# Kernel tuning notes

Hardware: AMD Instinct MI355X
Metric: run time of the kernel (lower is better)

## Reference

```python
import jax, jax.numpy as jnp
import numpy as np

N, E, C, Z, NB, NG, NL = 4000, 48000, 64, 10, 8, 8, 2
R_MAX = 5.0
P = 5.0  # polynomial cutoff power
AVG_NEIGH = 12.0
# l-index of each of the 16 spherical-harmonic components (l = 0..3)
ELLS = np.concatenate([[0], [1] * 3, [2] * 5, [3] * 7])


def _sph(u):
    # component-normalized real spherical harmonics up to l=3, u: unit vectors [E,3]
    x, y, z = u[..., 0], u[..., 1], u[..., 2]
    s3 = np.sqrt(3.0); s5 = np.sqrt(5.0); s15 = np.sqrt(15.0)
    s7 = np.sqrt(7.0); s105 = np.sqrt(105.0)
    s35_8 = np.sqrt(35.0 / 8.0); s21_8 = np.sqrt(21.0 / 8.0)
    x2, y2, z2 = x * x, y * y, z * z
    return jnp.stack([
        jnp.ones_like(x),
        s3 * x, s3 * y, s3 * z,
        s15 * x * y, s15 * y * z, 0.5 * s5 * (3.0 * z2 - 1.0), s15 * x * z, 0.5 * s15 * (x2 - y2),
        s35_8 * y * (3.0 * x2 - y2), s105 * x * y * z, s21_8 * y * (5.0 * z2 - 1.0),
        0.5 * s7 * z * (5.0 * z2 - 3.0), s21_8 * x * (5.0 * z2 - 1.0),
        0.5 * s105 * z * (x2 - y2), s35_8 * x * (x2 - 3.0 * y2),
    ], axis=-1)


def _radial(r):
    # Bessel radial basis * polynomial cutoff envelope; r: [E,1] -> [E,NB]
    n = jnp.arange(1, NB + 1, dtype=r.dtype)
    bess = np.sqrt(2.0 / R_MAX) * jnp.sin(n * jnp.pi * r / R_MAX) / r
    u = r / R_MAX
    env = 1.0 - 0.5 * (P + 1) * (P + 2) * u ** P + P * (P + 2) * u ** (P + 1) - 0.5 * P * (P + 1) * u ** (P + 2)
    env = jnp.where(u < 1.0, env, 0.0)
    return bess * env


def _per_l(f, W):
    # per-degree (l) channel mixing: f [N,C,16], W [4,C,C]
    return jnp.einsum('ncm,mcd->ndm', f, W[ELLS])


def _model(positions, x, shifts, W_embed, W_up, Wm1, Wm2, Wm3, W_out, W_sc, a_sc, w_poly, W_prod, w_r0, W_r1, w_r2, edge_index, batch):
    sender, receiver = edge_index[0], edge_index[1]
    vec = positions[receiver] - positions[sender] + shifts          # [E,3]
    length = jnp.sqrt(jnp.sum(vec * vec, axis=-1, keepdims=True))   # [E,1]
    edge_attrs = _sph(vec / length)                                 # [E,16]
    edge_feats = _radial(length)                                    # [E,NB]
    nf = jnp.zeros((N, C, 16), positions.dtype).at[:, :, 0].set(x @ W_embed)
    node_e = jnp.zeros((N,), positions.dtype)
    for i in range(NL):
        h = _per_l(nf, W_up[i])                                     # [N,C,16]
        w = jax.nn.silu(edge_feats @ Wm1[i])
        w = jax.nn.silu(w @ Wm2[i])
        w = (w @ Wm3[i]).reshape(E, C, 4)                           # per-(channel,l) radial weights
        h_s = h[:, :, 0][sender][:, :, None]                        # sender scalar feats [E,C,1]
        m = w[:, :, ELLS] * edge_attrs[:, None, :] * h_s            # messages [E,C,16]
        agg = jax.ops.segment_sum(m, receiver, num_segments=N) / AVG_NEIGH
        out = _per_l(agg, W_out[i])
        sc = _per_l(nf, W_sc[i]) * (x @ a_sc[i])[:, :, None]        # element-dependent skip
        s = out[:, :, 0]
        gate = w_poly[i, 0] + w_poly[i, 1] * s + w_poly[i, 2] * s * s  # correlation-3 scalar gate
        nf = _per_l(out * gate[:, :, None], W_prod[i]) + sc
        if i < NL - 1:
            node_e = node_e + nf[:, :, 0] @ w_r0
        else:
            node_e = node_e + jax.nn.silu(nf[:, :, 0] @ W_r1) @ w_r2
    snap = jax.ops.segment_sum(node_e, batch, num_segments=NG)
    return snap, node_e


def setup_inputs() -> dict:
    key = jax.random.key(0)
    ks = jax.random.split(key, 20)
    positions = jax.random.normal(ks[0], (N, 3), jnp.float32) * 3.0
    species = jax.random.randint(ks[1], (N,), 0, Z)
    x = jax.nn.one_hot(species, Z, dtype=jnp.float32)
    sender = jax.random.randint(ks[2], (E,), 0, N)
    offset = jax.random.randint(ks[3], (E,), 1, N)
    receiver = (sender + offset) % N  # no self loops -> length > 0
    edge_index = jnp.stack([sender, receiver]).astype(jnp.int32)
    shifts = jnp.zeros((E, 3), jnp.float32)
    batch = jnp.sort(jax.random.randint(ks[4], (N,), 0, NG)).astype(jnp.int32)
    g = lambda k, shp, scale: jax.random.normal(k, shp, jnp.float32) * scale
    inv = 1.0 / np.sqrt(C)
    return {
        'positions': positions, 'x': x, 'shifts': shifts,
        'W_embed': g(ks[5], (Z, C), 1.0 / np.sqrt(Z)),
        'W_up': g(ks[6], (NL, 4, C, C), inv),
        'Wm1': g(ks[7], (NL, NB, 64), 1.0 / np.sqrt(NB)),
        'Wm2': g(ks[8], (NL, 64, 64), 0.125),
        'Wm3': g(ks[9], (NL, 64, 4 * C), 0.125),
        'W_out': g(ks[10], (NL, 4, C, C), inv),
        'W_sc': g(ks[11], (NL, 4, C, C), inv),
        'a_sc': g(ks[12], (NL, Z, C), 1.0),
        'w_poly': g(ks[13], (NL, 3, C), 0.5),
        'W_prod': g(ks[14], (NL, 4, C, C), inv),
        'w_r0': g(ks[15], (C,), inv),
        'W_r1': g(ks[16], (C, 16), inv),
        'w_r2': g(ks[17], (16,), 0.25),
        'edge_index': edge_index, 'batch': batch,
    }


def reference(positions, x, shifts, W_embed, W_up, Wm1, Wm2, Wm3, W_out, W_sc, a_sc, w_poly, W_prod, w_r0, W_r1, w_r2, edge_index, batch):
    def efn(pos):
        snap, node_e = _model(pos, x, shifts, W_embed, W_up, Wm1, Wm2, Wm3, W_out, W_sc, a_sc, w_poly, W_prod, w_r0, W_r1, w_r2, edge_index, batch)
        return jnp.sum(snap), (snap, node_e)
    (_, (snap, node_e)), g = jax.value_and_grad(efn, has_aux=True)(positions)
    forces = -g
    return snap, node_e, forces
```

## Files before the change

kernel.cpp:

```cpp
#include <hip/hip_runtime.h>
#include <math.h>

constexpr int NN = 4000;
constexpr int EE = 48000;
constexpr int ZZ = 10;
constexpr float RMAX = 5.0f;
constexpr float INV_AVG = 1.0f / 12.0f;

constexpr int ZERO_F4 = (3*NN*64 + 3*NN + 4) / 4;

__device__ __forceinline__ float rl(float v, int lane){
    return __uint_as_float(__builtin_amdgcn_readlane(__float_as_uint(v), lane));
}
__device__ __forceinline__ float sigf(float x){ return 1.0f/(1.0f+__expf(-x)); }
__device__ __forceinline__ float siluf(float x){ return x*sigf(x); }
__device__ __forceinline__ float dsiluf(float x){ float s=sigf(x); return s*(1.0f+x*(1.0f-s)); }

__device__ __forceinline__ void pin64(float (&W)[64]){
#pragma unroll
    for (int i=0;i<64;i++) asm volatile("" : "+v"(W[i]));
}
__device__ __forceinline__ void pin8(float (&W)[8]){
#pragma unroll
    for (int i=0;i<8;i++) asm volatile("" : "+v"(W[i]));
}

__device__ __forceinline__ float bmv64(float src, const float (&W)[64]){
    float a0=0.f,a1=0.f,a2=0.f,a3=0.f;
#pragma unroll
    for (int k=0;k<64;k+=4){
        a0 += rl(src,k+0)*W[k+0];
        a1 += rl(src,k+1)*W[k+1];
        a2 += rl(src,k+2)*W[k+2];
        a3 += rl(src,k+3)*W[k+3];
    }
    return (a0+a1)+(a2+a3);
}
__device__ __forceinline__ void load_row64(const float* __restrict__ p, float (&W)[64]){
#pragma unroll
    for (int i=0;i<16;i++){
        float4 v = reinterpret_cast<const float4*>(p)[i];
        W[4*i]=v.x; W[4*i+1]=v.y; W[4*i+2]=v.z; W[4*i+3]=v.w;
    }
}
__device__ __forceinline__ void load_col64(const float* __restrict__ p, int lane, float (&W)[64]){
#pragma unroll
    for (int k=0;k<64;k++) W[k] = p[k*64+lane];
}

__global__ void k_zero(float4* __restrict__ z, float* __restrict__ out)
{
    int i = blockIdx.x*256 + threadIdx.x;
    if (i < ZERO_F4) z[i] = make_float4(0.f,0.f,0.f,0.f);
    if (blockIdx.x==0 && threadIdx.x<8) out[threadIdx.x] = 0.0f;
}

__global__ void k_geom(const float* __restrict__ pos, const float* __restrict__ shifts,
                       const int* __restrict__ ei, const float* __restrict__ x,
                       const float* __restrict__ WE, const float* __restrict__ W_up,
                       const float* __restrict__ W_sc, const float* __restrict__ a_sc,
                       const float* __restrict__ Wm3,
                       int* __restrict__ spec,
                       float* __restrict__ u3c, float* __restrict__ frc, float* __restrict__ dfrc,
                       int* __restrict__ esrc, int* __restrict__ edst, int* __restrict__ ecount,
                       float* __restrict__ T0, float* __restrict__ SC0, float* __restrict__ W3z)
{
    int b = blockIdx.x;
    if (b >= 236){
        int wv = (b-236)*4 + (threadIdx.x>>6);
        int lane = threadIdx.x & 63;
        if (wv < ZZ){
            float wev = WE[wv*64 + lane];
            float t=0.f, sc=0.f;
#pragma unroll
            for (int c=0;c<64;c++){
                float w = rl(wev,c);
                t  += w*W_up[c*64+lane];
                sc += w*W_sc[c*64+lane];
            }
            T0[wv*64+lane]  = t;
            SC0[wv*64+lane] = sc * a_sc[wv*64+lane];
        }
        return;
    }
    if (b >= 204){
        int idx = (b-204)*256 + threadIdx.x;
        int l = idx >> 12;
        int kc = idx & 4095;
        int k = kc >> 6, c = kc & 63;
        W3z[idx] = Wm3[l*64*256 + k*256 + 4*c];
        return;
    }
    if (b >= 188){
        int n = (b-188)*256 + threadIdx.x;
        if (n < NN){
            int sp = 0;
#pragma unroll
            for (int j=0;j<ZZ;j++) if (x[n*ZZ+j] > 0.5f) sp = j;
            spec[n] = sp;
        }
        return;
    }
    int e = b*256 + threadIdx.x;
    if (e >= EE) return;
    int s = ei[e], r = ei[EE+e];
    float vx = pos[r*3+0]-pos[s*3+0]+shifts[e*3+0];
    float vy = pos[r*3+1]-pos[s*3+1]+shifts[e*3+1];
    float vz = pos[r*3+2]-pos[s*3+2]+shifts[e*3+2];
    float rr = sqrtf(vx*vx+vy*vy+vz*vz);
    float u = rr*(1.0f/RMAX);
    if (u >= 1.0f) return;
    int slot = atomicAdd(ecount, 1);
    esrc[slot]=s; edst[slot]=r;
    float inv = 1.0f/rr;
    u3c[slot*3+0]=vx*inv; u3c[slot*3+1]=vy*inv; u3c[slot*3+2]=vz*inv;
    float u2=u*u, u4=u2*u2, u5=u4*u;
    float env  = 1.0f - 21.0f*u5 + 35.0f*u5*u - 15.0f*u5*u2;
    float om   = 1.0f-u;
    float denv = -21.0f*u4*om*om;
    const float A = 0.6324555320336759f;
    const float K1 = 3.14159265358979f/RMAX;
    float a  = K1*rr;
    float s1 = __sinf(a), c1 = __cosf(a);
    float sp = 0.0f, cp = 1.0f, sn = s1, cn = c1;
#pragma unroll
    for (int n=1;n<=8;n++){
        float k = (float)n*K1;
        float bess  = A*sn*inv;
        float dbess = A*(k*cn - sn*inv)*inv;
        frc [slot*8+n-1] = bess*env;
        dfrc[slot*8+n-1] = dbess*env + bess*denv;
        float s2 = 2.0f*c1*sn - sp; sp=sn; sn=s2;
        float c2 = 2.0f*c1*cn - cp; cp=cn; cn=c2;
    }
}

template<int L>
__global__ __launch_bounds__(256,3)
void k_edge_fwd(const float* __restrict__ frc, const int* __restrict__ esrc,
                const int* __restrict__ edst, const int* __restrict__ ecount,
                const int* __restrict__ spec, const float* __restrict__ T0,
                const float* __restrict__ h1,
                const float* __restrict__ W1, const float* __restrict__ W2,
                const float* __restrict__ W3z,
                float* __restrict__ agg, float* __restrict__ t2b,
                float* __restrict__ w0b)
{
    int lane = threadIdx.x & 63;
    int wid  = (blockIdx.x*256 + threadIdx.x) >> 6;
    int nw   = gridDim.x*4;
    int cnt  = ecount[0];
    float W1c[8], W2c[64], W3c[64];
#pragma unroll
    for (int j=0;j<8;j++) W1c[j] = W1[j*64+lane];
    load_col64(W2,  lane, W2c);
    load_col64(W3z, lane, W3c);
    pin8(W1c); pin64(W2c); pin64(W3c);
    for (int slot=wid; slot<cnt; slot+=nw){
        int us = __builtin_amdgcn_readfirstlane(slot);
        int s = esrc[us], r = edst[us];
        float fv = frc[us*8 + (lane&7)];
        float t1=0.f;
#pragma unroll
        for (int j=0;j<8;j++) t1 += rl(fv,j)*W1c[j];
        float a1v = siluf(t1);
        float t2  = bmv64(a1v, W2c);
        t2b[(size_t)us*64+lane] = t2;
        float a2v = siluf(t2);
        float w0  = bmv64(a2v, W3c);
        if (L==1) w0b[(size_t)us*64+lane] = w0;
        float h = (L==0) ? T0[spec[s]*64+lane] : h1[s*64+lane];
        atomicAdd(&agg[r*64+lane], w0*h*INV_AVG);
    }
}

__global__ __launch_bounds__(256,2)
void k_node_fwd0(const float* __restrict__ agg, const float* __restrict__ SC0,
                 const int* __restrict__ spec, const float* __restrict__ Wout,
                 const float* __restrict__ Wprod, const float* __restrict__ Wup1,
                 const float* __restrict__ poly, const float* __restrict__ wr0,
                 float* __restrict__ s0, float* __restrict__ nf1,
                 float* __restrict__ h1, float* __restrict__ nodee)
{
    int lane = threadIdx.x & 63;
    int wid = (blockIdx.x*256 + threadIdx.x) >> 6;
    int nw  = gridDim.x*4;
    float Oc[64], Pc[64], Uc[64];
    load_col64(Wout, lane, Oc);
    load_col64(Wprod,lane, Pc);
    load_col64(Wup1, lane, Uc);
    pin64(Oc); pin64(Pc); pin64(Uc);
    float p0=poly[lane], p1=poly[64+lane], p2=poly[128+lane];
    float w0r = wr0[lane];
    for (int nn=wid; nn<NN; nn+=nw){
        int n = __builtin_amdgcn_readfirstlane(nn);
        float av = agg[n*64+lane];
        float s  = bmv64(av, Oc);
        float gate = p0 + p1*s + p2*s*s;
        float v  = s*gate;
        float nf = bmv64(v, Pc) + SC0[spec[n]*64+lane];
        s0 [n*64+lane] = s;
        nf1[n*64+lane] = nf;
        h1 [n*64+lane] = bmv64(nf, Uc);
        float ne = nf*w0r;
#pragma unroll
        for (int off=32;off;off>>=1) ne += __shfl_xor(ne,off);
        if (lane==0) nodee[n] = ne;
    }
}

__global__ __launch_bounds__(256,2)
void k_node_fwd1(const float* __restrict__ agg, const float* __restrict__ nf1,
                 const int* __restrict__ spec, const float* __restrict__ Wout,
                 const float* __restrict__ Wprod, const float* __restrict__ Wsc,
                 const float* __restrict__ asc, const float* __restrict__ poly,
                 float* __restrict__ s1, float* __restrict__ nf2)
{
    int lane = threadIdx.x & 63;
    int wid = (blockIdx.x*256 + threadIdx.x) >> 6;
    int nw  = gridDim.x*4;
    float Oc[64], Pc[64], Sc[64];
    load_col64(Wout, lane, Oc);
    load_col64(Wprod,lane, Pc);
    load_col64(Wsc,  lane, Sc);
    pin64(Oc); pin64(Pc); pin64(Sc);
    float p0=poly[lane], p1=poly[64+lane], p2=poly[128+lane];
    for (int nn=wid; nn<NN; nn+=nw){
        int n = __builtin_amdgcn_readfirstlane(nn);
        float av  = agg[n*64+lane];
        float nfv = nf1[n*64+lane];
        float s   = bmv64(av, Oc);
        float gate = p0 + p1*s + p2*s*s;
        float v   = s*gate;
        float scp = bmv64(nfv, Sc);
        float nf  = bmv64(v, Pc) + scp*asc[spec[n]*64+lane];
        s1 [n*64+lane] = s;
        nf2[n*64+lane] = nf;
    }
}

__global__ __launch_bounds__(256,3)
void k_read1(const float* __restrict__ nf2, const float* __restrict__ Wr1,
             const float* __restrict__ wr2, float* __restrict__ nodee,
             float* __restrict__ gnf2)
{
    int lane = threadIdx.x & 63;
    int wid = (blockIdx.x*256 + threadIdx.x) >> 6;
    int nw  = gridDim.x*4;
    int j = lane & 15;
    float Wcol[64];
#pragma unroll
    for (int c=0;c<64;c++) Wcol[c] = Wr1[c*16 + j];
    pin64(Wcol);
    float Wrow[16];
#pragma unroll
    for (int i=0;i<4;i++){
        float4 v = reinterpret_cast<const float4*>(Wr1 + lane*16)[i];
        Wrow[4*i]=v.x; Wrow[4*i+1]=v.y; Wrow[4*i+2]=v.z; Wrow[4*i+3]=v.w;
    }
    float w2 = wr2[j];
    for (int nn=wid; nn<NN; nn+=nw){
        int n = __builtin_amdgcn_readfirstlane(nn);
        float nv = nf2[n*64+lane];
        float z  = bmv64(nv, Wcol);
        float ne = siluf(z)*w2;
#pragma unroll
        for (int off=32;off;off>>=1) ne += __shfl_xor(ne,off);
        ne *= 0.25f;
        float gz = w2*dsiluf(z);
        float g = 0.f;
#pragma unroll
        for (int jj=0;jj<16;jj++) g += rl(gz,jj)*Wrow[jj];
        gnf2[n*64+lane] = g;
        if (lane==0) nodee[n] += ne;
    }
}

__global__ __launch_bounds__(256,2)
void k_bnode1(const float* __restrict__ gin, const float* __restrict__ sbuf,
              const float* __restrict__ Wout, const float* __restrict__ Wprod,
              const float* __restrict__ Wsc, const float* __restrict__ asc,
              const int* __restrict__ spec, const float* __restrict__ poly,
              float* __restrict__ gagg, float* __restrict__ gsc)
{
    int lane = threadIdx.x & 63;
    int wid = (blockIdx.x*256 + threadIdx.x) >> 6;
    int nw  = gridDim.x*4;
    float Pr[64], Or[64], Sr[64];
    load_row64(Wprod + lane*64, Pr);
    load_row64(Wout  + lane*64, Or);
    load_row64(Wsc   + lane*64, Sr);
    pin64(Pr); pin64(Or); pin64(Sr);
    float p0=poly[lane], p1=poly[64+lane], p2=poly[128+lane];
    for (int nn=wid; nn<NN; nn+=nw){
        int n = __builtin_amdgcn_readfirstlane(nn);
        float g  = gin[n*64+lane];
        float gv = bmv64(g, Pr);
        float s  = sbuf[n*64+lane];
        float gate = p0 + p1*s + p2*s*s;
        float gs = gv*(gate + s*(p1 + 2.0f*p2*s));
        gagg[n*64+lane] = bmv64(gs, Or);
        float ga = g * asc[spec[n]*64+lane];
        gsc[n*64+lane] = bmv64(ga, Sr);
    }
}

__global__ __launch_bounds__(256,2)
void k_bnode0(const float* __restrict__ ghb, const float* __restrict__ gacc,
              const float* __restrict__ Wup1, const float* __restrict__ wr0,
              const float* __restrict__ sbuf, const float* __restrict__ Wout,
              const float* __restrict__ Wprod, const float* __restrict__ poly,
              float* __restrict__ gagg)
{
    int lane = threadIdx.x & 63;
    int wid = (blockIdx.x*256 + threadIdx.x) >> 6;
    int nw  = gridDim.x*4;
    float Ur[64], Pr[64], Or[64];
    load_row64(Wup1 + lane*64, Ur);
    load_row64(Wprod+ lane*64, Pr);
    load_row64(Wout + lane*64, Or);
    pin64(Ur); pin64(Pr); pin64(Or);
    float p0=poly[lane], p1=poly[64+lane], p2=poly[128+lane];
    for (int nn=wid; nn<NN; nn+=nw){
        int n = __builtin_amdgcn_readfirstlane(nn);
        float gh = ghb[n*64+lane];
        float g  = bmv64(gh, Ur) + gacc[n*64+lane] + wr0[lane];
        float gv = bmv64(g, Pr);
        float s  = sbuf[n*64+lane];
        float gate = p0 + p1*s + p2*s*s;
        float gs = gv*(gate + s*(p1 + 2.0f*p2*s));
        gagg[n*64+lane] = bmv64(gs, Or);
    }
}

template<int L>
__global__ __launch_bounds__(256,3)
void k_edge_bwd(const float* __restrict__ frc, const float* __restrict__ dfrc,
                const float* __restrict__ u3c, const int* __restrict__ esrc,
                const int* __restrict__ edst, const int* __restrict__ ecount,
                const int* __restrict__ spec, const float* __restrict__ T0,
                const float* __restrict__ h1, const float* __restrict__ gagg,
                const float* __restrict__ t2b, const float* __restrict__ w0b,
                const float* __restrict__ W1, const float* __restrict__ W2,
                const float* __restrict__ W3z,
                float* __restrict__ ghb, float* __restrict__ gpos)
{
    int lane = threadIdx.x & 63;
    int wid  = (blockIdx.x*256 + threadIdx.x) >> 6;
    int nw   = gridDim.x*4;
    int cnt  = ecount[0];
    float W3r[64], W2r[64], W1c[8];
    load_row64(W3z + lane*64, W3r);
    load_row64(W2  + lane*64, W2r);
#pragma unroll
    for (int j=0;j<8;j++) W1c[j] = W1[j*64+lane];
    pin64(W3r); pin64(W2r); pin8(W1c);
    for (int slot=wid; slot<cnt; slot+=nw){
        int us = __builtin_amdgcn_readfirstlane(slot);
        int s = esrc[us], r = edst[us];
        float gm = gagg[r*64+lane]*INV_AVG;
        float h  = (L==0) ? T0[spec[s]*64+lane] : h1[s*64+lane];
        float gw0 = gm*h;
        if (L==1) atomicAdd(&ghb[s*64+lane], gm*w0b[(size_t)us*64+lane]);
        float ga2 = bmv64(gw0, W3r);
        float t2v = t2b[(size_t)us*64+lane];
        float gt2 = ga2*dsiluf(t2v);
        float ga1 = bmv64(gt2, W2r);
        float fv  = frc [us*8+(lane&7)];
        float dfv = dfrc[us*8+(lane&7)];
        float t1=0.f, wd=0.f;
#pragma unroll
        for (int j=0;j<8;j++){ t1 += rl(fv,j)*W1c[j]; wd += rl(dfv,j)*W1c[j]; }
        float gt1 = ga1*dsiluf(t1);
        float p = gt1*wd;
#pragma unroll
        for (int off=32;off;off>>=1) p += __shfl_xor(p,off);
        if (lane<3) atomicAdd(&gpos[r*3+lane],  u3c[us*3+lane]*p);
        else if (lane>=32 && lane<35){ int d=lane-32; atomicAdd(&gpos[s*3+d], -u3c[us*3+d]*p); }
    }
}

__global__ void k_final(const float* __restrict__ node_e, const int* __restrict__ batch,
                        const float* __restrict__ gpos, float* __restrict__ out)
{
    __shared__ float part[8];
    int tid=threadIdx.x;
    if (tid<8) part[tid]=0.0f;
    __syncthreads();
    int n = blockIdx.x*256 + tid;
    if (n<NN){
        float ne = node_e[n];
        out[8+n] = ne;
        atomicAdd(&part[batch[n]], ne);
        out[8+NN + n*3+0] = -gpos[n*3+0];
        out[8+NN + n*3+1] = -gpos[n*3+1];
        out[8+NN + n*3+2] = -gpos[n*3+2];
    }
    __syncthreads();
    if (tid<8) atomicAdd(&out[tid], part[tid]);
}

extern "C" void kernel_launch(void* const* d_in, const int* in_sizes, int n_in,
                              void* d_out, int out_size, void* d_ws, size_t ws_size,
                              hipStream_t stream)
{
    (void)in_sizes; (void)n_in; (void)out_size; (void)ws_size;
    const float* pos    = (const float*)d_in[0];
    const float* x      = (const float*)d_in[1];
    const float* shifts = (const float*)d_in[2];
    const float* W_embed= (const float*)d_in[3];
    const float* W_up   = (const float*)d_in[4];
    const float* Wm1    = (const float*)d_in[5];
    const float* Wm2    = (const float*)d_in[6];
    const float* Wm3    = (const float*)d_in[7];
    const float* W_out  = (const float*)d_in[8];
    const float* W_sc   = (const float*)d_in[9];
    const float* a_sc   = (const float*)d_in[10];
    const float* w_poly = (const float*)d_in[11];
    const float* W_prod = (const float*)d_in[12];
    const float* w_r0   = (const float*)d_in[13];
    const float* W_r1   = (const float*)d_in[14];
    const float* w_r2   = (const float*)d_in[15];
    const int*   ei     = (const int*)d_in[16];
    const int*   batch  = (const int*)d_in[17];
    float* out = (float*)d_out;

    float* F = (float*)d_ws;
    float* agg0 = F; F += NN*64;
    float* agg1 = F; F += NN*64;
    float* ghb  = F; F += NN*64;
    float* gpos = F; F += NN*3;
    int* ecount = (int*)F; F += 4;
    float* u3c  = F; F += 3*EE;
    float* frc  = F; F += 8*EE;
    float* dfrc = F; F += 8*EE;
    float* t2b0 = F; F += (size_t)EE*64;
    float* t2b1 = F; F += (size_t)EE*64;
    float* w0b1 = F; F += (size_t)EE*64;
    float* h1   = F; F += NN*64;
    float* nf1  = F; F += NN*64;
    float* nf2  = F; F += NN*64;
    float* s0   = F; F += NN*64;
    float* s1   = F; F += NN*64;
    float* nodee= F; F += NN;
    float* gnf2 = F; F += NN*64;
    float* gagg1= F; F += NN*64;
    float* gagg0= F; F += NN*64;
    float* gacc = F; F += NN*64;
    float* T0   = F; F += ZZ*64;
    float* SC0  = F; F += ZZ*64;
    float* W3z  = F; F += 2*64*64;
    int* spec   = (int*)F; F += NN;
    int* esrc   = (int*)F; F += EE;
    int* edst   = (int*)F; F += EE;

    const float* U0 = W_up;           const float* U1 = W_up   + 4*64*64;
    const float* O0 = W_out;          const float* O1 = W_out  + 4*64*64;
    const float* S0w= W_sc;           const float* S1w= W_sc   + 4*64*64;
    const float* P0 = W_prod;         const float* P1 = W_prod + 4*64*64;
    const float* M1_0=Wm1,  *M1_1=Wm1+8*64;
    const float* M2_0=Wm2,  *M2_1=Wm2+64*64;
    const float* asc1=a_sc+ZZ*64;
    const float* pl0=w_poly, *pl1=w_poly+3*64;
    float* W3z0 = W3z; float* W3z1 = W3z + 64*64;

    k_zero<<<(ZERO_F4+255)/256, 256, 0, stream>>>((float4*)d_ws, out);
    k_geom<<<239, 256, 0, stream>>>(pos, shifts, ei, x, W_embed, U0, S0w, a_sc, Wm3,
                                    spec, u3c, frc, dfrc, esrc, edst, ecount, T0, SC0, W3z);

    k_edge_fwd<0><<<768,256,0,stream>>>(frc, esrc, edst, ecount, spec, T0, nullptr,
                                        M1_0, M2_0, W3z0, agg0, t2b0, nullptr);
    k_node_fwd0<<<500,256,0,stream>>>(agg0, SC0, spec, O0, P0, U1, pl0, w_r0,
                                      s0, nf1, h1, nodee);
    k_edge_fwd<1><<<768,256,0,stream>>>(frc, esrc, edst, ecount, spec, nullptr, h1,
                                        M1_1, M2_1, W3z1, agg1, t2b1, w0b1);
    k_node_fwd1<<<500,256,0,stream>>>(agg1, nf1, spec, O1, P1, S1w, asc1, pl1, s1, nf2);
    k_read1<<<500,256,0,stream>>>(nf2, W_r1, w_r2, nodee, gnf2);

    k_bnode1<<<500,256,0,stream>>>(gnf2, s1, O1, P1, S1w, asc1, spec, pl1, gagg1, gacc);
    k_edge_bwd<1><<<768,256,0,stream>>>(frc, dfrc, u3c, esrc, edst, ecount, spec, nullptr, h1,
                                        gagg1, t2b1, w0b1, M1_1, M2_1, W3z1, ghb, gpos);
    k_bnode0<<<500,256,0,stream>>>(ghb, gacc, U1, w_r0, s0, O0, P0, pl0, gagg0);
    k_edge_bwd<0><<<768,256,0,stream>>>(frc, dfrc, u3c, esrc, edst, ecount, spec, T0, nullptr,
                                        gagg0, t2b0, nullptr, M1_0, M2_0, W3z0, nullptr, gpos);

    k_final<<<16,256,0,stream>>>(nodee, batch, gpos, out);
}
```

Baseline: 150.9 us.

## Fuse node kernels, fold zeroing and final pass, recompute layer-0 edge MLP

Several changes land together. Workspace zeroing moves into extra blocks of the geometry kernel, and the final output kernel is removed: forces accumulate straight into the output and node energies reduce per graph inside the node kernels. The layer-1 node forward, readout and backward node kernels merge into one with four nodes per wave. Layer-0 edge backward recomputes the hidden activation instead of storing and reloading a 48000x64 buffer, and edge and node grids shrink. This cuts launches and memory traffic at the cost of extra recompute, higher register pressure and more atomics to the output.

```diff
diff --git a/kernel.cpp b/kernel.cpp
--- a/kernel.cpp
+++ b/kernel.cpp
@@ -7,7 +7,13 @@
 constexpr float RMAX = 5.0f;
 constexpr float INV_AVG = 1.0f / 12.0f;
 
-constexpr int ZERO_F4 = (3*NN*64 + 3*NN + 4) / 4;
+constexpr int GB_EDGE = 188;
+constexpr int GB_SPEC = GB_EDGE + 16;
+constexpr int GB_W3Z  = GB_SPEC + 32;
+constexpr int GB_T0   = GB_W3Z + 3;
+constexpr int GB_ZERO = GB_T0 + 64;
+constexpr int ZWS_F4  = 3*NN*64/4;
+constexpr int ZOUT_F4 = 3*NN/4;
 
 __device__ __forceinline__ float rl(float v, int lane){
     return __uint_as_float(__builtin_amdgcn_readlane(__float_as_uint(v), lane));
@@ -48,11 +54,11 @@
     for (int k=0;k<64;k++) W[k] = p[k*64+lane];
 }
 
-__global__ void k_zero(float4* __restrict__ z, float* __restrict__ out)
-{
-    int i = blockIdx.x*256 + threadIdx.x;
-    if (i < ZERO_F4) z[i] = make_float4(0.f,0.f,0.f,0.f);
-    if (blockIdx.x==0 && threadIdx.x<8) out[threadIdx.x] = 0.0f;
+__global__ void k_zero(int* __restrict__ ecount, float* __restrict__ out)
+{
+    int t = threadIdx.x;
+    if (t < 8) out[t] = 0.0f;
+    if (t == 8) *ecount = 0;
 }
 
 __global__ void k_geom(const float* __restrict__ pos, const float* __restrict__ shifts,
@@ -63,11 +69,25 @@
                        int* __restrict__ spec,
                        float* __restrict__ u3c, float* __restrict__ frc, float* __restrict__ dfrc,
                        int* __restrict__ esrc, int* __restrict__ edst, int* __restrict__ ecount,
-                       float* __restrict__ T0, float* __restrict__ SC0, float* __restrict__ W3z)
+                       float* __restrict__ T0, float* __restrict__ SC0, float* __restrict__ W3z,
+                       float4* __restrict__ zws, float* __restrict__ out)
 {
     int b = blockIdx.x;
-    if (b >= 236){
-        int wv = (b-236)*4 + (threadIdx.x>>6);
+    if (b >= GB_T0){
+        if (b >= GB_ZERO) return;
+        if (b >= GB_W3Z && b < GB_T0){}
+        if (b >= GB_T0 && b < GB_ZERO){
+            float4 z4 = make_float4(0.f,0.f,0.f,0.f);
+            float4* zout = (float4*)(out + 8 + NN);
+            for (int i=(b-GB_T0)*256 + threadIdx.x; i < ZWS_F4 + ZOUT_F4; i += 64*256){
+                if (i < ZWS_F4) zws[i] = z4;
+                else zout[i-ZWS_F4] = z4;
+            }
+            return;
+        }
+    }
+    if (b >= GB_W3Z && b < GB_T0){
+        int wv = (b-GB_W3Z)*4 + (threadIdx.x>>6);
         int lane = threadIdx.x & 63;
         if (wv < ZZ){
             float wev = WE[wv*64 + lane];
@@ -83,16 +103,16 @@
         }
         return;
     }
-    if (b >= 204){
-        int idx = (b-204)*256 + threadIdx.x;
+    if (b >= GB_SPEC && b < GB_W3Z){
+        int idx = (b-GB_SPEC)*256 + threadIdx.x;
         int l = idx >> 12;
         int kc = idx & 4095;
         int k = kc >> 6, c = kc & 63;
         W3z[idx] = Wm3[l*64*256 + k*256 + 4*c];
         return;
     }
-    if (b >= 188){
-        int n = (b-188)*256 + threadIdx.x;
+    if (b >= GB_EDGE){
+        int n = (b-GB_EDGE)*256 + threadIdx.x;
         if (n < NN){
             int sp = 0;
 #pragma unroll
@@ -147,8 +167,8 @@
                 float* __restrict__ w0b)
 {
     int lane = threadIdx.x & 63;
-    int wid  = (blockIdx.x*256 + threadIdx.x) >> 6;
-    int nw   = gridDim.x*4;
+    int wid  = __builtin_amdgcn_readfirstlane((blockIdx.x*256 + threadIdx.x) >> 6);
+    const int nw = 512*4;
     int cnt  = ecount[0];
     float W1c[8], W2c[64], W3c[64];
 #pragma unroll
@@ -165,10 +185,12 @@
         for (int j=0;j<8;j++) t1 += rl(fv,j)*W1c[j];
         float a1v = siluf(t1);
         float t2  = bmv64(a1v, W2c);
-        t2b[(size_t)us*64+lane] = t2;
         float a2v = siluf(t2);
         float w0  = bmv64(a2v, W3c);
-        if (L==1) w0b[(size_t)us*64+lane] = w0;
+        if (L==1){
+            t2b[(size_t)us*64+lane] = t2;
+            w0b[(size_t)us*64+lane] = w0;
+        }
         float h = (L==0) ? T0[spec[s]*64+lane] : h1[s*64+lane];
         atomicAdd(&agg[r*64+lane], w0*h*INV_AVG);
     }
@@ -176,93 +198,91 @@
 
 __global__ __launch_bounds__(256,2)
 void k_node_fwd0(const float* __restrict__ agg, const float* __restrict__ SC0,
-                 const int* __restrict__ spec, const float* __restrict__ Wout,
-                 const float* __restrict__ Wprod, const float* __restrict__ Wup1,
-                 const float* __restrict__ poly, const float* __restrict__ wr0,
+                 const int* __restrict__ spec, const int* __restrict__ batch,
+                 const float* __restrict__ Wout, const float* __restrict__ Wprod,
+                 const float* __restrict__ Wup1, const float* __restrict__ poly,
+                 const float* __restrict__ wr0,
                  float* __restrict__ s0, float* __restrict__ nf1,
-                 float* __restrict__ h1, float* __restrict__ nodee)
-{
+                 float* __restrict__ h1, float* __restrict__ out)
+{
+    __shared__ float part[8];
+    if (threadIdx.x < 8) part[threadIdx.x] = 0.f;
+    __syncthreads();
     int lane = threadIdx.x & 63;
-    int wid = (blockIdx.x*256 + threadIdx.x) >> 6;
-    int nw  = gridDim.x*4;
-    float Oc[64], Pc[64], Uc[64];
-    load_col64(Wout, lane, Oc);
-    load_col64(Wprod,lane, Pc);
-    load_col64(Wup1, lane, Uc);
-    pin64(Oc); pin64(Pc); pin64(Uc);
+    int wid = __builtin_amdgcn_readfirstlane((blockIdx.x*256 + threadIdx.x) >> 6);
+    float WA[64], WB[64], WC[64];
+    load_col64(Wout, lane, WA);
+    load_col64(Wprod,lane, WB);
+    load_col64(Wup1, lane, WC);
+    pin64(WA); pin64(WB); pin64(WC);
     float p0=poly[lane], p1=poly[64+lane], p2=poly[128+lane];
     float w0r = wr0[lane];
-    for (int nn=wid; nn<NN; nn+=nw){
-        int n = __builtin_amdgcn_readfirstlane(nn);
+#pragma unroll
+    for (int i=0;i<4;i++){
+        int n = wid + i*1000;
         float av = agg[n*64+lane];
-        float s  = bmv64(av, Oc);
+        float s  = bmv64(av, WA);
         float gate = p0 + p1*s + p2*s*s;
-        float v  = s*gate;
-        float nf = bmv64(v, Pc) + SC0[spec[n]*64+lane];
+        float nf = bmv64(s*gate, WB) + SC0[spec[n]*64+lane];
         s0 [n*64+lane] = s;
         nf1[n*64+lane] = nf;
-        h1 [n*64+lane] = bmv64(nf, Uc);
+        h1 [n*64+lane] = bmv64(nf, WC);
         float ne = nf*w0r;
 #pragma unroll
         for (int off=32;off;off>>=1) ne += __shfl_xor(ne,off);
-        if (lane==0) nodee[n] = ne;
-    }
+        if (lane==0){ out[8+n] = ne; atomicAdd(&part[batch[n]], ne); }
+    }
+    __syncthreads();
+    if (threadIdx.x < 8) atomicAdd(&out[threadIdx.x], part[threadIdx.x]);
 }
 
 __global__ __launch_bounds__(256,2)
-void k_node_fwd1(const float* __restrict__ agg, const float* __restrict__ nf1,
-                 const int* __restrict__ spec, const float* __restrict__ Wout,
-                 const float* __restrict__ Wprod, const float* __restrict__ Wsc,
-                 const float* __restrict__ asc, const float* __restrict__ poly,
-                 float* __restrict__ s1, float* __restrict__ nf2)
-{
+void k_node1(const float* __restrict__ agg, const float* __restrict__ nf1,
+             const int* __restrict__ spec, const int* __restrict__ batch,
+             const float* __restrict__ Wout, const float* __restrict__ Wprod,
+             const float* __restrict__ Wsc, const float* __restrict__ asc,
+             const float* __restrict__ poly, const float* __restrict__ Wr1,
+             const float* __restrict__ wr2,
+             float* __restrict__ out, float* __restrict__ gagg, float* __restrict__ gacc)
+{
+    __shared__ float part[8];
+    if (threadIdx.x < 8) part[threadIdx.x] = 0.f;
+    __syncthreads();
     int lane = threadIdx.x & 63;
-    int wid = (blockIdx.x*256 + threadIdx.x) >> 6;
-    int nw  = gridDim.x*4;
-    float Oc[64], Pc[64], Sc[64];
-    load_col64(Wout, lane, Oc);
-    load_col64(Wprod,lane, Pc);
-    load_col64(Wsc,  lane, Sc);
-    pin64(Oc); pin64(Pc); pin64(Sc);
+    int wid = __builtin_amdgcn_readfirstlane((blockIdx.x*256 + threadIdx.x) >> 6);
+    float WA[64], WB[64], WC[64];
+    float sA[4], nfA[4], gA[4]; int spA[4];
     float p0=poly[lane], p1=poly[64+lane], p2=poly[128+lane];
-    for (int nn=wid; nn<NN; nn+=nw){
-        int n = __builtin_amdgcn_readfirstlane(nn);
+    load_col64(Wout, lane, WA);
+    load_col64(Wprod,lane, WB);
+    load_col64(Wsc,  lane, WC);
+    pin64(WA); pin64(WB); pin64(WC);
+#pragma unroll
+    for (int i=0;i<4;i++){
+        int n = wid + i*1000;
+        spA[i] = spec[n];
         float av  = agg[n*64+lane];
         float nfv = nf1[n*64+lane];
-        float s   = bmv64(av, Oc);
+        float s   = bmv64(av, WA);
         float gate = p0 + p1*s + p2*s*s;
-        float v   = s*gate;
-        float scp = bmv64(nfv, Sc);
-        float nf  = bmv64(v, Pc) + scp*asc[spec[n]*64+lane];
-        s1 [n*64+lane] = s;
-        nf2[n*64+lane] = nf;
-    }
-}
-
-__global__ __launch_bounds__(256,3)
-void k_read1(const float* __restrict__ nf2, const float* __restrict__ Wr1,
-             const float* __restrict__ wr2, float* __restrict__ nodee,
-             float* __restrict__ gnf2)
-{
-    int lane = threadIdx.x & 63;
-    int wid = (blockIdx.x*256 + threadIdx.x) >> 6;
-    int nw  = gridDim.x*4;
+        float scp = bmv64(nfv, WC);
+        sA[i]  = s;
+        nfA[i] = bmv64(s*gate, WB) + scp*asc[spA[i]*64+lane];
+    }
     int j = lane & 15;
-    float Wcol[64];
-#pragma unroll
-    for (int c=0;c<64;c++) Wcol[c] = Wr1[c*16 + j];
-    pin64(Wcol);
-    float Wrow[16];
+    float w2 = wr2[j];
+#pragma unroll
+    for (int c=0;c<64;c++) WA[c] = Wr1[c*16 + j];
+    pin64(WA);
+#pragma unroll
+    for (int i2=0;i2<4;i2++){
+        float4 v = reinterpret_cast<const float4*>(Wr1 + lane*16)[i2];
+        WC[4*i2]=v.x; WC[4*i2+1]=v.y; WC[4*i2+2]=v.z; WC[4*i2+3]=v.w;
+    }
 #pragma unroll
     for (int i=0;i<4;i++){
-        float4 v = reinterpret_cast<const float4*>(Wr1 + lane*16)[i];
-        Wrow[4*i]=v.x; Wrow[4*i+1]=v.y; Wrow[4*i+2]=v.z; Wrow[4*i+3]=v.w;
-    }
-    float w2 = wr2[j];
-    for (int nn=wid; nn<NN; nn+=nw){
-        int n = __builtin_amdgcn_readfirstlane(nn);
-        float nv = nf2[n*64+lane];
-        float z  = bmv64(nv, Wcol);
+        int n = wid + i*1000;
+        float z  = bmv64(nfA[i], WA);
         float ne = siluf(z)*w2;
 #pragma unroll
         for (int off=32;off;off>>=1) ne += __shfl_xor(ne,off);
@@ -270,39 +290,27 @@
         float gz = w2*dsiluf(z);
         float g = 0.f;
 #pragma unroll
-        for (int jj=0;jj<16;jj++) g += rl(gz,jj)*Wrow[jj];
-        gnf2[n*64+lane] = g;
-        if (lane==0) nodee[n] += ne;
-    }
-}
-
-__global__ __launch_bounds__(256,2)
-void k_bnode1(const float* __restrict__ gin, const float* __restrict__ sbuf,
-              const float* __restrict__ Wout, const float* __restrict__ Wprod,
-              const float* __restrict__ Wsc, const float* __restrict__ asc,
-              const int* __restrict__ spec, const float* __restrict__ poly,
-              float* __restrict__ gagg, float* __restrict__ gsc)
-{
-    int lane = threadIdx.x & 63;
-    int wid = (blockIdx.x*256 + threadIdx.x) >> 6;
-    int nw  = gridDim.x*4;
-    float Pr[64], Or[64], Sr[64];
-    load_row64(Wprod + lane*64, Pr);
-    load_row64(Wout  + lane*64, Or);
-    load_row64(Wsc   + lane*64, Sr);
-    pin64(Pr); pin64(Or); pin64(Sr);
-    float p0=poly[lane], p1=poly[64+lane], p2=poly[128+lane];
-    for (int nn=wid; nn<NN; nn+=nw){
-        int n = __builtin_amdgcn_readfirstlane(nn);
-        float g  = gin[n*64+lane];
-        float gv = bmv64(g, Pr);
-        float s  = sbuf[n*64+lane];
+        for (int jj=0;jj<16;jj++) g += rl(gz,jj)*WC[jj];
+        gA[i] = g;
+        if (lane==0){ out[8+n] += ne; atomicAdd(&part[batch[n]], ne); }
+    }
+    load_row64(Wprod + lane*64, WA);
+    load_row64(Wout  + lane*64, WB);
+    load_row64(Wsc   + lane*64, WC);
+    pin64(WA); pin64(WB); pin64(WC);
+#pragma unroll
+    for (int i=0;i<4;i++){
+        int n = wid + i*1000;
+        float g  = gA[i];
+        float gv = bmv64(g, WA);
+        float s  = sA[i];
         float gate = p0 + p1*s + p2*s*s;
         float gs = gv*(gate + s*(p1 + 2.0f*p2*s));
-        gagg[n*64+lane] = bmv64(gs, Or);
-        float ga = g * asc[spec[n]*64+lane];
-        gsc[n*64+lane] = bmv64(ga, Sr);
-    }
+        gagg[n*64+lane] = bmv64(gs, WB);
+        gacc[n*64+lane] = bmv64(g*asc[spA[i]*64+lane], WC);
+    }
+    __syncthreads();
+    if (threadIdx.x < 8) atomicAdd(&out[threadIdx.x], part[threadIdx.x]);
 }
 
 __global__ __launch_bounds__(256,2)
@@ -313,42 +321,42 @@
               float* __restrict__ gagg)
 {
     int lane = threadIdx.x & 63;
-    int wid = (blockIdx.x*256 + threadIdx.x) >> 6;
-    int nw  = gridDim.x*4;
-    float Ur[64], Pr[64], Or[64];
-    load_row64(Wup1 + lane*64, Ur);
-    load_row64(Wprod+ lane*64, Pr);
-    load_row64(Wout + lane*64, Or);
-    pin64(Ur); pin64(Pr); pin64(Or);
+    int wid = __builtin_amdgcn_readfirstlane((blockIdx.x*256 + threadIdx.x) >> 6);
+    float WA[64], WB[64], WC[64];
+    load_row64(Wup1 + lane*64, WA);
+    load_row64(Wprod+ lane*64, WB);
+    load_row64(Wout + lane*64, WC);
+    pin64(WA); pin64(WB); pin64(WC);
     float p0=poly[lane], p1=poly[64+lane], p2=poly[128+lane];
-    for (int nn=wid; nn<NN; nn+=nw){
-        int n = __builtin_amdgcn_readfirstlane(nn);
+    float w0r = wr0[lane];
+#pragma unroll
+    for (int i=0;i<4;i++){
+        int n = wid + i*1000;
         float gh = ghb[n*64+lane];
-        float g  = bmv64(gh, Ur) + gacc[n*64+lane] + wr0[lane];
-        float gv = bmv64(g, Pr);
+        float g  = bmv64(gh, WA) + gacc[n*64+lane] + w0r;
+        float gv = bmv64(g, WB);
         float s  = sbuf[n*64+lane];
         float gate = p0 + p1*s + p2*s*s;
         float gs = gv*(gate + s*(p1 + 2.0f*p2*s));
-        gagg[n*64+lane] = bmv64(gs, Or);
-    }
-}
-
-template<int L>
+        gagg[n*64+lane] = bmv64(gs, WC);
+    }
+}
+
 __global__ __launch_bounds__(256,3)
-void k_edge_bwd(const float* __restrict__ frc, const float* __restrict__ dfrc,
-                const float* __restrict__ u3c, const int* __restrict__ esrc,
-                const int* __restrict__ edst, const int* __restrict__ ecount,
-                const int* __restrict__ spec, const float* __restrict__ T0,
-                const float* __restrict__ h1, const float* __restrict__ gagg,
-                const float* __restrict__ t2b, const float* __restrict__ w0b,
-                const float* __restrict__ W1, const float* __restrict__ W2,
-                const float* __restrict__ W3z,
-                float* __restrict__ ghb, float* __restrict__ gpos)
+void k_edge_bwd1(const float* __restrict__ frc, const float* __restrict__ dfrc,
+                 const float* __restrict__ u3c, const int* __restrict__ esrc,
+                 const int* __restrict__ edst, const int* __restrict__ ecount,
+                 const float* __restrict__ h1, const float* __restrict__ gagg,
+                 const float* __restrict__ t2b, const float* __restrict__ w0b,
+                 const float* __restrict__ W1, const float* __restrict__ W2,
+                 const float* __restrict__ W3z,
+                 float* __restrict__ ghb, float* __restrict__ out)
 {
     int lane = threadIdx.x & 63;
-    int wid  = (blockIdx.x*256 + threadIdx.x) >> 6;
-    int nw   = gridDim.x*4;
+    int wid  = __builtin_amdgcn_readfirstlane((blockIdx.x*256 + threadIdx.x) >> 6);
+    const int nw = 512*4;
     int cnt  = ecount[0];
+    float* outf = out + 8 + NN;
     float W3r[64], W2r[64], W1c[8];
     load_row64(W3z + lane*64, W3r);
     load_row64(W2  + lane*64, W2r);
@@ -359,45 +367,67 @@
         int us = __builtin_amdgcn_readfirstlane(slot);
         int s = esrc[us], r = edst[us];
         float gm = gagg[r*64+lane]*INV_AVG;
-        float h  = (L==0) ? T0[spec[s]*64+lane] : h1[s*64+lane];
-        float gw0 = gm*h;
-        if (L==1) atomicAdd(&ghb[s*64+lane], gm*w0b[(size_t)us*64+lane]);
-        float ga2 = bmv64(gw0, W3r);
-        float t2v = t2b[(size_t)us*64+lane];
-        float gt2 = ga2*dsiluf(t2v);
+        float h  = h1[s*64+lane];
+        atomicAdd(&ghb[s*64+lane], gm*w0b[(size_t)us*64+lane]);
+        float ga2 = bmv64(gm*h, W3r);
+        float gt2 = ga2*dsiluf(t2b[(size_t)us*64+lane]);
         float ga1 = bmv64(gt2, W2r);
         float fv  = frc [us*8+(lane&7)];
         float dfv = dfrc[us*8+(lane&7)];
         float t1=0.f, wd=0.f;
 #pragma unroll
         for (int j=0;j<8;j++){ t1 += rl(fv,j)*W1c[j]; wd += rl(dfv,j)*W1c[j]; }
-        float gt1 = ga1*dsiluf(t1);
-        float p = gt1*wd;
+        float p = ga1*dsiluf(t1)*wd;
 #pragma unroll
         for (int off=32;off;off>>=1) p += __shfl_xor(p,off);
-        if (lane<3) atomicAdd(&gpos[r*3+lane],  u3c[us*3+lane]*p);
-        else if (lane>=32 && lane<35){ int d=lane-32; atomicAdd(&gpos[s*3+d], -u3c[us*3+d]*p); }
-    }
-}
-
-__global__ void k_final(const float* __restrict__ node_e, const int* __restrict__ batch,
-                        const float* __restrict__ gpos, float* __restrict__ out)
-{
-    __shared__ float part[8];
-    int tid=threadIdx.x;
-    if (tid<8) part[tid]=0.0f;
-    __syncthreads();
-    int n = blockIdx.x*256 + tid;
-    if (n<NN){
-        float ne = node_e[n];
-        out[8+n] = ne;
-        atomicAdd(&part[batch[n]], ne);
-        out[8+NN + n*3+0] = -gpos[n*3+0];
-        out[8+NN + n*3+1] = -gpos[n*3+1];
-        out[8+NN + n*3+2] = -gpos[n*3+2];
-    }
-    __syncthreads();
-    if (tid<8) atomicAdd(&out[tid], part[tid]);
+        if (lane<3) atomicAdd(&outf[r*3+lane], -u3c[us*3+lane]*p);
+        else if (lane>=32 && lane<35){ int d=lane-32; atomicAdd(&outf[s*3+d], u3c[us*3+d]*p); }
+    }
+}
+
+__global__ __launch_bounds__(256,2)
+void k_edge_bwd0(const float* __restrict__ frc, const float* __restrict__ dfrc,
+                 const float* __restrict__ u3c, const int* __restrict__ esrc,
+                 const int* __restrict__ edst, const int* __restrict__ ecount,
+                 const int* __restrict__ spec, const float* __restrict__ T0,
+                 const float* __restrict__ gagg,
+                 const float* __restrict__ W1, const float* __restrict__ W2,
+                 const float* __restrict__ W3z,
+                 float* __restrict__ out)
+{
+    int lane = threadIdx.x & 63;
+    int wid  = __builtin_amdgcn_readfirstlane((blockIdx.x*256 + threadIdx.x) >> 6);
+    const int nw = 512*4;
+    int cnt  = ecount[0];
+    float* outf = out + 8 + NN;
+    float W3r[64], W2r[64], W2c[64], W1c[8];
+    load_row64(W3z + lane*64, W3r);
+    load_row64(W2  + lane*64, W2r);
+    load_col64(W2, lane, W2c);
+#pragma unroll
+    for (int j=0;j<8;j++) W1c[j] = W1[j*64+lane];
+    pin64(W3r); pin64(W2r); pin64(W2c); pin8(W1c);
+    for (int slot=wid; slot<cnt; slot+=nw){
+        int us = __builtin_amdgcn_readfirstlane(slot);
+        int s = esrc[us], r = edst[us];
+        float gm = gagg[r*64+lane]*INV_AVG;
+        float h  = T0[spec[s]*64+lane];
+        float ga2 = bmv64(gm*h, W3r);
+        float fv  = frc [us*8+(lane&7)];
+        float dfv = dfrc[us*8+(lane&7)];
+        float t1=0.f, wd=0.f;
+#pragma unroll
+        for (int j=0;j<8;j++){ t1 += rl(fv,j)*W1c[j]; wd += rl(dfv,j)*W1c[j]; }
+        float a1v = siluf(t1);
+        float t2  = bmv64(a1v, W2c);
+        float gt2 = ga2*dsiluf(t2);
+        float ga1 = bmv64(gt2, W2r);
+        float p = ga1*dsiluf(t1)*wd;
+#pragma unroll
+        for (int off=32;off;off>>=1) p += __shfl_xor(p,off);
+        if (lane<3) atomicAdd(&outf[r*3+lane], -u3c[us*3+lane]*p);
+        else if (lane>=32 && lane<35){ int d=lane-32; atomicAdd(&outf[s*3+d], u3c[us*3+d]*p); }
+    }
 }
 
 extern "C" void kernel_launch(void* const* d_in, const int* in_sizes, int n_in,
@@ -429,21 +459,15 @@
     float* agg0 = F; F += NN*64;
     float* agg1 = F; F += NN*64;
     float* ghb  = F; F += NN*64;
-    float* gpos = F; F += NN*3;
     int* ecount = (int*)F; F += 4;
     float* u3c  = F; F += 3*EE;
     float* frc  = F; F += 8*EE;
     float* dfrc = F; F += 8*EE;
-    float* t2b0 = F; F += (size_t)EE*64;
     float* t2b1 = F; F += (size_t)EE*64;
     float* w0b1 = F; F += (size_t)EE*64;
     float* h1   = F; F += NN*64;
     float* nf1  = F; F += NN*64;
-    float* nf2  = F; F += NN*64;
     float* s0   = F; F += NN*64;
-    float* s1   = F; F += NN*64;
-    float* nodee= F; F += NN;
-    float* gnf2 = F; F += NN*64;
     float* gagg1= F; F += NN*64;
     float* gagg0= F; F += NN*64;
     float* gacc = F; F += NN*64;
@@ -464,25 +488,23 @@
     const float* pl0=w_poly, *pl1=w_poly+3*64;
     float* W3z0 = W3z; float* W3z1 = W3z + 64*64;
 
-    k_zero<<<(ZERO_F4+255)/256, 256, 0, stream>>>((float4*)d_ws, out);
-    k_geom<<<239, 256, 0, stream>>>(pos, shifts, ei, x, W_embed, U0, S0w, a_sc, Wm3,
-                                    spec, u3c, frc, dfrc, esrc, edst, ecount, T0, SC0, W3z);
-
-    k_edge_fwd<0><<<768,256,0,stream>>>(frc, esrc, edst, ecount, spec, T0, nullptr,
-                                        M1_0, M2_0, W3z0, agg0, t2b0, nullptr);
-    k_node_fwd0<<<500,256,0,stream>>>(agg0, SC0, spec, O0, P0, U1, pl0, w_r0,
-                                      s0, nf1, h1, nodee);
-    k_edge_fwd<1><<<768,256,0,stream>>>(frc, esrc, edst, ecount, spec, nullptr, h1,
+    k_zero<<<1, 256, 0, stream>>>(ecount, out);
+    k_geom<<<GB_ZERO, 256, 0, stream>>>(pos, shifts, ei, x, W_embed, U0, S0w, a_sc, Wm3,
+                                        spec, u3c, frc, dfrc, esrc, edst, ecount,
+                                        T0, SC0, W3z, (float4*)d_ws, out);
+
+    k_edge_fwd<0><<<512,256,0,stream>>>(frc, esrc, edst, ecount, spec, T0, nullptr,
+                                        M1_0, M2_0, W3z0, agg0, nullptr, nullptr);
+    k_node_fwd0<<<250,256,0,stream>>>(agg0, SC0, spec, batch, O0, P0, U1, pl0, w_r0,
+                                      s0, nf1, h1, out);
+    k_edge_fwd<1><<<512,256,0,stream>>>(frc, esrc, edst, ecount, spec, nullptr, h1,
                                         M1_1, M2_1, W3z1, agg1, t2b1, w0b1);
-    k_node_fwd1<<<500,256,0,stream>>>(agg1, nf1, spec, O1, P1, S1w, asc1, pl1, s1, nf2);
-    k_read1<<<500,256,0,stream>>>(nf2, W_r1, w_r2, nodee, gnf2);
-
-    k_bnode1<<<500,256,0,stream>>>(gnf2, s1, O1, P1, S1w, asc1, spec, pl1, gagg1, gacc);
-    k_edge_bwd<1><<<768,256,0,stream>>>(frc, dfrc, u3c, esrc, edst, ecount, spec, nullptr, h1,
-                                        gagg1, t2b1, w0b1, M1_1, M2_1, W3z1, ghb, gpos);
-    k_bnode0<<<500,256,0,stream>>>(ghb, gacc, U1, w_r0, s0, O0, P0, pl0, gagg0);
-    k_edge_bwd<0><<<768,256,0,stream>>>(frc, dfrc, u3c, esrc, edst, ecount, spec, T0, nullptr,
-                                        gagg0, t2b0, nullptr, M1_0, M2_0, W3z0, nullptr, gpos);
-
-    k_final<<<16,256,0,stream>>>(nodee, batch, gpos, out);
-}
+    k_node1<<<250,256,0,stream>>>(agg1, nf1, spec, batch, O1, P1, S1w, asc1, pl1,
+                                  W_r1, w_r2, out, gagg1, gacc);
+
+    k_edge_bwd1<<<512,256,0,stream>>>(frc, dfrc, u3c, esrc, edst, ecount, h1,
+                                      gagg1, t2b1, w0b1, M1_1, M2_1, W3z1, ghb, out);
+    k_bnode0<<<250,256,0,stream>>>(ghb, gacc, U1, w_r0, s0, O0, P0, pl0, gagg0);
+    k_edge_bwd0<<<512,256,0,stream>>>(frc, dfrc, u3c, esrc, edst, ecount, spec, T0,
+                                      gagg0, M1_0, M2_0, W3z0, out);
+}
```

Measured after the change: 159.3 us. 5.6% more time.
